# Optimization experiments

Hardware: AMD Instinct MI355X
Metric: run time of the kernel (lower is better)

The kernel has to match this reference:

```python
import jax, jax.numpy as jnp
import numpy as np

LN_EPS = 1e-5

def _layernorm(x, g, b):
    mu = jnp.mean(x, axis=-1, keepdims=True)
    var = jnp.mean(jnp.square(x - mu), axis=-1, keepdims=True)
    return (x - mu) * jax.lax.rsqrt(var + LN_EPS) * g + b

def setup_inputs() -> dict:
    key = jax.random.key(0)
    B, IN_DIM, S, D = 16384, 512, 32, 128
    ks = jax.random.split(key, 6)
    return {
        "x": jax.random.normal(ks[0], (B, IN_DIM), dtype=jnp.float32),
        "memory": jax.random.normal(ks[1], (1, S, D), dtype=jnp.float32),
        "ln_g": jnp.ones((IN_DIM,), dtype=jnp.float32),
        "ln_b": jnp.zeros((IN_DIM,), dtype=jnp.float32),
        "w_in": jax.random.normal(ks[2], (IN_DIM, D), dtype=jnp.float32) * 0.02,
        "b_in": jnp.zeros((D,), dtype=jnp.float32),
        "w_gate": jax.random.normal(ks[3], (2 * D, D), dtype=jnp.float32) * 0.02,
        "b_gate": jnp.zeros((D,), dtype=jnp.float32),
    }

def reference(x, memory, ln_g, ln_b, w_in, b_in, w_gate, b_gate):
    B = x.shape[0]
    mem = memory[0]                                   # [S, D]
    S, D = mem.shape
    x_proj = _layernorm(x, ln_g, ln_b) @ w_in + b_in  # [B, D]
    scores = x_proj @ mem.T                           # [B, S]
    probs = jax.nn.softmax(scores, axis=-1)           # [B, S]
    # read path
    read_content = probs @ mem                        # [B, D]
    # write path
    mem_b = jnp.broadcast_to(mem, (B, S, D))
    xp_b = jnp.broadcast_to(x_proj[:, None, :], (B, S, D))
    gate_in = jnp.concatenate([mem_b, xp_b], axis=-1)              # [B, S, 2D]
    update_gate = jax.nn.sigmoid(gate_in @ w_gate + b_gate)        # [B, S, D]
    write_info = probs[:, :, None] * x_proj[:, None, :]            # [B, S, D]
    avg_gate = jnp.mean(update_gate, axis=0, keepdims=True)        # [1, S, D]
    avg_write = jnp.mean(write_info, axis=0, keepdims=True)        # [1, S, D]
    new_memory = memory * (1.0 - avg_gate) + avg_write * avg_gate  # [1, S, D]
    return read_content, jax.lax.stop_gradient(new_memory)
```

## Files before the change

kernel.cpp:

```cpp
#include <hip/hip_runtime.h>
#include <stdint.h>

typedef __attribute__((ext_vector_type(8))) short bfrag_t;
typedef __attribute__((ext_vector_type(4))) float floatx4;

#define WFRAG_OFF   0
#define GB_OFF      294912
#define BU_OFF      311296
#define BS_OFF      311808
#define MEMFRAG_OFF 311936
#define ACC_OFF     327680
#define NBLK        512

#define M_A     0
#define M_XPF   32768
#define M_U     40960
#define M_SC    57344
#define M_PR    61440
#define M_PRT   63488
#define M_LDS   65536

__device__ __forceinline__ unsigned short f2bf(float f) {
    unsigned u = __float_as_uint(f);
    u += 0x7fffu + ((u >> 16) & 1u);
    return (unsigned short)(u >> 16);
}
__device__ __forceinline__ float sigm(float v) {
    return __builtin_amdgcn_rcpf(1.0f + __expf(-v));
}
__device__ __forceinline__ void writefrag(unsigned short* wf, int k, int n, float v) {
    int kt = k >> 5, kk = k & 31;
    int lane = (n & 15) | ((kk >> 3) << 4);
    wf[(((kt * 18) + (n >> 4)) * 64 + lane) * 8 + (kk & 7)] = f2bf(v);
}

__global__ __launch_bounds__(256) void prep_kernel(
    const float* __restrict__ memv, const float* __restrict__ w_in,
    const float* __restrict__ b_in, const float* __restrict__ w_gate,
    const float* __restrict__ b_gate, unsigned char* __restrict__ ws)
{
    int bid = blockIdx.x, t = threadIdx.x;
    unsigned short* wfrag = (unsigned short*)(ws + WFRAG_OFF);
    const float* wg2 = w_gate + 128 * 128;

    if (bid < 256) {
        __shared__ float wrow[2][128];
        int k0 = bid * 2;
        wrow[t >> 7][t & 127] = w_in[(size_t)(k0 + (t >> 7)) * 128 + (t & 127)];
        __syncthreads();
        for (int kl = 0; kl < 2; ++kl) {
            int k = k0 + kl;
            float v;
            if (t < 128) {
                v = wrow[kl][t];
            } else {
                int d = t - 128;
                float acc = 0.f;
                #pragma unroll 16
                for (int j = 0; j < 128; ++j) acc += wrow[kl][j] * wg2[j * 128 + d];
                v = acc;
            }
            writefrag(wfrag, k, t, v);
            if (t < 32) {
                float acc = 0.f;
                #pragma unroll 16
                for (int d = 0; d < 128; ++d) acc += wrow[kl][d] * memv[t * 128 + d];
                writefrag(wfrag, k, 256 + t, acc);
            }
        }
    } else if (bid < 272) {
        int idx = (bid - 256) * 256 + t;
        int s = idx >> 7, d = idx & 127;
        float acc = b_gate[d];
        #pragma unroll 16
        for (int k = 0; k < 128; ++k) acc += memv[s * 128 + k] * w_gate[k * 128 + d];
        ((float*)(ws + GB_OFF))[idx] = acc;
    } else {
        if (t < 128) {
            float acc = 0.f;
            #pragma unroll 16
            for (int j = 0; j < 128; ++j) acc += b_in[j] * wg2[j * 128 + t];
            ((float*)(ws + BU_OFF))[t] = acc;
        }
        if (t < 32) {
            float acc = 0.f;
            #pragma unroll 16
            for (int d = 0; d < 128; ++d) acc += b_in[d] * memv[t * 128 + d];
            ((float*)(ws + BS_OFF))[t] = acc;
        }
        unsigned short* mfr = (unsigned short*)(ws + MEMFRAG_OFF);
        for (int idx = t; idx < 4096; idx += 256) {
            int s = idx >> 7, d = idx & 127;
            mfr[((d >> 4) * 64 + ((d & 15) | (((s >> 3) & 3) << 4))) * 8 + (s & 7)]
                = f2bf(memv[idx]);
        }
    }
}

__global__ __launch_bounds__(512, 4) void main_kernel(
    const float* __restrict__ x,
    const float* __restrict__ ln_g, const float* __restrict__ ln_b,
    const float* __restrict__ b_in, unsigned char* __restrict__ ws,
    float* __restrict__ out)
{
    __shared__ char smem[M_LDS] __attribute__((aligned(16)));

    int tid = threadIdx.x;
    int w = tid >> 6, l = tid & 63;
    int lane_lo = l & 15, lane_hi = l >> 4;
    int row_base = blockIdx.x * 32;

    const float4* x4 = (const float4*)x;
    float4 g0 = ((const float4*)ln_g)[l];
    float4 g1 = ((const float4*)ln_g)[l + 64];
    float4 q0 = ((const float4*)ln_b)[l];
    float4 q1 = ((const float4*)ln_b)[l + 64];
    #pragma unroll
    for (int i = 0; i < 4; ++i) {
        int r = w * 4 + i;
        float4 xa = x4[(size_t)(row_base + r) * 128 + l];
        float4 xb = x4[(size_t)(row_base + r) * 128 + 64 + l];
        float s1 = xa.x + xa.y + xa.z + xa.w + xb.x + xb.y + xb.z + xb.w;
        float s2 = xa.x*xa.x + xa.y*xa.y + xa.z*xa.z + xa.w*xa.w
                 + xb.x*xb.x + xb.y*xb.y + xb.z*xb.z + xb.w*xb.w;
        #pragma unroll
        for (int m = 1; m < 64; m <<= 1) {
            s1 += __shfl_xor(s1, m);
            s2 += __shfl_xor(s2, m);
        }
        float mu = s1 * (1.f / 512.f);
        float var = s2 * (1.f / 512.f) - mu * mu;
        float rs = rsqrtf(var + 1e-5f);
        float ya0 = (xa.x - mu) * rs * g0.x + q0.x;
        float ya1 = (xa.y - mu) * rs * g0.y + q0.y;
        float ya2 = (xa.z - mu) * rs * g0.z + q0.z;
        float ya3 = (xa.w - mu) * rs * g0.w + q0.w;
        float yb0 = (xb.x - mu) * rs * g1.x + q1.x;
        float yb1 = (xb.y - mu) * rs * g1.y + q1.y;
        float yb2 = (xb.z - mu) * rs * g1.z + q1.z;
        float yb3 = (xb.w - mu) * rs * g1.w + q1.w;
        unsigned long long pa =
            (unsigned long long)f2bf(ya0) | ((unsigned long long)f2bf(ya1) << 16) |
            ((unsigned long long)f2bf(ya2) << 32) | ((unsigned long long)f2bf(ya3) << 48);
        unsigned long long pb =
            (unsigned long long)f2bf(yb0) | ((unsigned long long)f2bf(yb1) << 16) |
            ((unsigned long long)f2bf(yb2) << 32) | ((unsigned long long)f2bf(yb3) << 48);
        int sw = (r & 7) << 4;
        *(unsigned long long*)(smem + M_A + ((r * 1024 + l * 8) ^ sw)) = pa;
        *(unsigned long long*)(smem + M_A + ((r * 1024 + 512 + l * 8) ^ sw)) = pb;
    }
    __syncthreads();

    int nf = (w < 2) ? 3 : 2;
    int nts[3] = {w, w + 8, 16 + w};

    const bfrag_t* wf = (const bfrag_t*)(ws + WFRAG_OFF);
    int swa = (l & 7) << 4;
    int ab0 = lane_lo * 1024 + (lane_hi << 4);
    int ab1 = (16 + lane_lo) * 1024 + (lane_hi << 4);

    floatx4 acc[3][2];
    #pragma unroll
    for (int i = 0; i < 3; ++i)
        #pragma unroll
        for (int mt = 0; mt < 2; ++mt)
            acc[i][mt] = (floatx4){0.f, 0.f, 0.f, 0.f};

    bfrag_t acur0, acur1, anxt0, anxt1, bcur[3], bnxt[3];
    acur0 = *(const bfrag_t*)(smem + M_A + (ab0 ^ swa));
    acur1 = *(const bfrag_t*)(smem + M_A + (ab1 ^ swa));
    #pragma unroll
    for (int i = 0; i < 3; ++i)
        if (i < nf) bcur[i] = wf[(0 * 18 + nts[i]) * 64 + l];

    for (int kt = 0; kt < 16; ++kt) {
        if (kt < 15) {
            int ko = (kt + 1) * 64;
            anxt0 = *(const bfrag_t*)(smem + M_A + ((ab0 + ko) ^ swa));
            anxt1 = *(const bfrag_t*)(smem + M_A + ((ab1 + ko) ^ swa));
            #pragma unroll
            for (int i = 0; i < 3; ++i)
                if (i < nf) bnxt[i] = wf[((kt + 1) * 18 + nts[i]) * 64 + l];
        }
        #pragma unroll
        for (int i = 0; i < 3; ++i) {
            if (i < nf) {
                acc[i][0] = __builtin_amdgcn_mfma_f32_16x16x32_bf16(acur0, bcur[i], acc[i][0], 0, 0, 0);
                acc[i][1] = __builtin_amdgcn_mfma_f32_16x16x32_bf16(acur1, bcur[i], acc[i][1], 0, 0, 0);
            }
        }
        acur0 = anxt0; acur1 = anxt1;
        #pragma unroll
        for (int i = 0; i < 3; ++i)
            if (i < nf) bcur[i] = bnxt[i];
    }

    {
        const float* bu = (const float*)(ws + BU_OFF);
        const float* bs = (const float*)(ws + BS_OFF);
        #pragma unroll
        for (int i = 0; i < 3; ++i) {
            if (i < nf) {
                int n = nts[i] * 16 + lane_lo;
                #pragma unroll
                for (int mt = 0; mt < 2; ++mt) {
                    #pragma unroll
                    for (int r4 = 0; r4 < 4; ++r4) {
                        int row = mt * 16 + lane_hi * 4 + r4;
                        float v = acc[i][mt][r4];
                        if (i == 0) {
                            float val = v + b_in[n];
                            int addr = M_XPF +
                                (((n >> 4) * 64 + ((n & 15) | ((row >> 3) << 4))) * 8
                                 + (row & 7)) * 2;
                            *(unsigned short*)(smem + addr) = f2bf(val);
                        } else if (i == 1) {
                            int d = n - 128;
                            *(float*)(smem + M_U + (row * 128 + d) * 4) = v + bu[d];
                        } else {
                            int s = n - 256;
                            *(float*)(smem + M_SC + (row * 32 + s) * 4) = v + bs[s];
                        }
                    }
                }
            }
        }
    }
    __syncthreads();

    #pragma unroll
    for (int i = 0; i < 4; ++i) {
        int r = w * 4 + i;
        int s = l & 31;
        float sc = *(const float*)(smem + M_SC + (r * 32 + s) * 4);
        float mx = sc;
        #pragma unroll
        for (int m = 1; m < 32; m <<= 1) mx = fmaxf(mx, __shfl_xor(mx, m));
        float e = __expf(sc - mx);
        float sum = e;
        #pragma unroll
        for (int m = 1; m < 32; m <<= 1) sum += __shfl_xor(sum, m);
        float p = e * __builtin_amdgcn_rcpf(sum);
        if (l < 32) {
            unsigned short pb = f2bf(p);
            *(unsigned short*)(smem + M_PR +
                (((r >> 4) * 64 + ((r & 15) + 16 * (s >> 3))) * 8 + (s & 7)) * 2) = pb;
            *(unsigned short*)(smem + M_PRT +
                (((s >> 4) * 64 + ((s & 15) + 16 * (r >> 3))) * 8 + (r & 7)) * 2) = pb;
        }
    }
    __syncthreads();

    float* pw = (float*)(ws + ACC_OFF + (size_t)blockIdx.x * 32768);
    {
        bfrag_t pa0 = *(const bfrag_t*)(smem + M_PR + l * 16);
        bfrag_t pa1 = *(const bfrag_t*)(smem + M_PR + 1024 + l * 16);
        bfrag_t pat0 = *(const bfrag_t*)(smem + M_PRT + l * 16);
        bfrag_t pat1 = *(const bfrag_t*)(smem + M_PRT + 1024 + l * 16);
        bfrag_t bm = ((const bfrag_t*)(ws + MEMFRAG_OFF))[w * 64 + l];
        bfrag_t bx = *(const bfrag_t*)(smem + M_XPF + (w * 64 + l) * 16);

        floatx4 r0 = (floatx4){0.f, 0.f, 0.f, 0.f};
        floatx4 r1 = (floatx4){0.f, 0.f, 0.f, 0.f};
        r0 = __builtin_amdgcn_mfma_f32_16x16x32_bf16(pa0, bm, r0, 0, 0, 0);
        r1 = __builtin_amdgcn_mfma_f32_16x16x32_bf16(pa1, bm, r1, 0, 0, 0);
        floatx4 w0 = (floatx4){0.f, 0.f, 0.f, 0.f};
        floatx4 w1 = (floatx4){0.f, 0.f, 0.f, 0.f};
        w0 = __builtin_amdgcn_mfma_f32_16x16x32_bf16(pat0, bx, w0, 0, 0, 0);
        w1 = __builtin_amdgcn_mfma_f32_16x16x32_bf16(pat1, bx, w1, 0, 0, 0);

        int nc = w * 16 + lane_lo;
        #pragma unroll
        for (int r4 = 0; r4 < 4; ++r4) {
            int row = lane_hi * 4 + r4;
            out[(size_t)(row_base + row) * 128 + nc] = r0[r4];
            out[(size_t)(row_base + row + 16) * 128 + nc] = r1[r4];
            pw[row * 128 + nc] = w0[r4];
            pw[(row + 16) * 128 + nc] = w1[r4];
        }
    }

    {
        int sbase = w * 4;
        const float* gb = (const float*)(ws + GB_OFF);
        float* pg = pw + 4096;
        float gbr0[4], gbr1[4], ag0[4], ag1[4];
        #pragma unroll
        for (int si = 0; si < 4; ++si) {
            gbr0[si] = gb[(sbase + si) * 128 + l];
            gbr1[si] = gb[(sbase + si) * 128 + l + 64];
            ag0[si] = 0.f; ag1[si] = 0.f;
        }
        for (int r = 0; r < 32; ++r) {
            float uv0 = *(const float*)(smem + M_U + (r * 128 + l) * 4);
            float uv1 = *(const float*)(smem + M_U + (r * 128 + l + 64) * 4);
            #pragma unroll
            for (int si = 0; si < 4; ++si) {
                ag0[si] += sigm(gbr0[si] + uv0);
                ag1[si] += sigm(gbr1[si] + uv1);
            }
        }
        #pragma unroll
        for (int si = 0; si < 4; ++si) {
            pg[(sbase + si) * 128 + l]      = ag0[si];
            pg[(sbase + si) * 128 + l + 64] = ag1[si];
        }
    }
}

__global__ __launch_bounds__(512) void fin_kernel(
    const float* __restrict__ memv, const unsigned char* __restrict__ ws,
    float* __restrict__ out2)
{
    __shared__ float4 red[2][32][16];
    int b = blockIdx.x, t = threadIdx.x;
    int f4 = t & 15, ch = t >> 4;
    const float* base = (const float*)(ws + ACC_OFF);
    int e4 = b * 16 + f4;

    float4 aw = {0.f, 0.f, 0.f, 0.f}, ag = {0.f, 0.f, 0.f, 0.f};
    #pragma unroll 4
    for (int c = ch * 16; c < ch * 16 + 16; ++c) {
        float4 a = ((const float4*)(base + (size_t)c * 8192))[e4];
        float4 g = ((const float4*)(base + (size_t)c * 8192 + 4096))[e4];
        aw.x += a.x; aw.y += a.y; aw.z += a.z; aw.w += a.w;
        ag.x += g.x; ag.y += g.y; ag.z += g.z; ag.w += g.w;
    }
    red[0][ch][f4] = aw;
    red[1][ch][f4] = ag;
    __syncthreads();
    if (t < 16) {
        float4 a = {0.f, 0.f, 0.f, 0.f}, g = {0.f, 0.f, 0.f, 0.f};
        #pragma unroll
        for (int c = 0; c < 32; ++c) {
            float4 ra = red[0][c][t], rg = red[1][c][t];
            a.x += ra.x; a.y += ra.y; a.z += ra.z; a.w += ra.w;
            g.x += rg.x; g.y += rg.y; g.z += rg.z; g.w += rg.w;
        }
        const float4 m4 = ((const float4*)memv)[b * 16 + t];
        float4 o;
        float s = 1.f / 16384.f;
        float gx = g.x * s, gy = g.y * s, gz = g.z * s, gw = g.w * s;
        o.x = m4.x * (1.f - gx) + a.x * s * gx;
        o.y = m4.y * (1.f - gy) + a.y * s * gy;
        o.z = m4.z * (1.f - gz) + a.z * s * gz;
        o.w = m4.w * (1.f - gw) + a.w * s * gw;
        ((float4*)out2)[b * 16 + t] = o;
    }
}

extern "C" void kernel_launch(void* const* d_in, const int* in_sizes, int n_in,
                              void* d_out, int out_size, void* d_ws, size_t ws_size,
                              hipStream_t stream)
{
    (void)in_sizes; (void)n_in; (void)out_size; (void)ws_size;
    const float* x      = (const float*)d_in[0];
    const float* memv   = (const float*)d_in[1];
    const float* ln_g   = (const float*)d_in[2];
    const float* ln_b   = (const float*)d_in[3];
    const float* w_in   = (const float*)d_in[4];
    const float* b_in   = (const float*)d_in[5];
    const float* w_gate = (const float*)d_in[6];
    const float* b_gate = (const float*)d_in[7];
    float* out = (float*)d_out;
    unsigned char* ws = (unsigned char*)d_ws;

    hipLaunchKernelGGL(prep_kernel, dim3(273), dim3(256), 0, stream,
                       memv, w_in, b_in, w_gate, b_gate, ws);
    hipLaunchKernelGGL(main_kernel, dim3(NBLK), dim3(512), 0, stream,
                       x, ln_g, ln_b, b_in, ws, out);
    hipLaunchKernelGGL(fin_kernel, dim3(64), dim3(512), 0, stream,
                       memv, ws, out + 2097152);
}
```

Measured before the change: 48.69 us.

## Hoist global loads earlier and deepen MFMA operand prefetch to two stages

Issues all x row loads up front, then prefetches the first two weight fragments and the bias values before the layernorm math, so global latency overlaps the reductions. The GEMM loop now prefetches both A and B fragments two k-steps ahead instead of one. The memory fragment, xproj fragment and gate-bias loads are hoisted above the softmax phase, and the sigmoid accumulation loop is unrolled by 4. This raises register pressure under launch_bounds(512,4), which could cause spills or lower occupancy.

Measured after the change: 49.15 us. No clear change (+0.9%).

```diff
diff --git a/kernel.cpp b/kernel.cpp
--- a/kernel.cpp
+++ b/kernel.cpp
@@ -110,19 +110,42 @@
     int lane_lo = l & 15, lane_hi = l >> 4;
     int row_base = blockIdx.x * 32;
 
+    int nf = (w < 2) ? 3 : 2;
+    int nts[3] = {w, w + 8, 16 + w};
+    const bfrag_t* wf = (const bfrag_t*)(ws + WFRAG_OFF);
+
     const float4* x4 = (const float4*)x;
     float4 g0 = ((const float4*)ln_g)[l];
     float4 g1 = ((const float4*)ln_g)[l + 64];
     float4 q0 = ((const float4*)ln_b)[l];
     float4 q1 = ((const float4*)ln_b)[l + 64];
+
+    float4 xa[4], xb[4];
     #pragma unroll
     for (int i = 0; i < 4; ++i) {
         int r = w * 4 + i;
-        float4 xa = x4[(size_t)(row_base + r) * 128 + l];
-        float4 xb = x4[(size_t)(row_base + r) * 128 + 64 + l];
-        float s1 = xa.x + xa.y + xa.z + xa.w + xb.x + xb.y + xb.z + xb.w;
-        float s2 = xa.x*xa.x + xa.y*xa.y + xa.z*xa.z + xa.w*xa.w
-                 + xb.x*xb.x + xb.y*xb.y + xb.z*xb.z + xb.w*xb.w;
+        xa[i] = x4[(size_t)(row_base + r) * 128 + l];
+        xb[i] = x4[(size_t)(row_base + r) * 128 + 64 + l];
+    }
+
+    bfrag_t bcur[3], bnxt[3], bfar[3];
+    #pragma unroll
+    for (int i = 0; i < 3; ++i) {
+        if (i < nf) {
+            bcur[i] = wf[(0 * 18 + nts[i]) * 64 + l];
+            bnxt[i] = wf[(1 * 18 + nts[i]) * 64 + l];
+        }
+    }
+    float bin_v = b_in[w * 16 + lane_lo];
+    float bu_v  = ((const float*)(ws + BU_OFF))[w * 16 + lane_lo];
+    float bs_v  = (w < 2) ? ((const float*)(ws + BS_OFF))[w * 16 + lane_lo] : 0.f;
+
+    #pragma unroll
+    for (int i = 0; i < 4; ++i) {
+        int r = w * 4 + i;
+        float s1 = xa[i].x + xa[i].y + xa[i].z + xa[i].w + xb[i].x + xb[i].y + xb[i].z + xb[i].w;
+        float s2 = xa[i].x*xa[i].x + xa[i].y*xa[i].y + xa[i].z*xa[i].z + xa[i].w*xa[i].w
+                 + xb[i].x*xb[i].x + xb[i].y*xb[i].y + xb[i].z*xb[i].z + xb[i].w*xb[i].w;
         #pragma unroll
         for (int m = 1; m < 64; m <<= 1) {
             s1 += __shfl_xor(s1, m);
@@ -131,14 +154,14 @@
         float mu = s1 * (1.f / 512.f);
         float var = s2 * (1.f / 512.f) - mu * mu;
         float rs = rsqrtf(var + 1e-5f);
-        float ya0 = (xa.x - mu) * rs * g0.x + q0.x;
-        float ya1 = (xa.y - mu) * rs * g0.y + q0.y;
-        float ya2 = (xa.z - mu) * rs * g0.z + q0.z;
-        float ya3 = (xa.w - mu) * rs * g0.w + q0.w;
-        float yb0 = (xb.x - mu) * rs * g1.x + q1.x;
-        float yb1 = (xb.y - mu) * rs * g1.y + q1.y;
-        float yb2 = (xb.z - mu) * rs * g1.z + q1.z;
-        float yb3 = (xb.w - mu) * rs * g1.w + q1.w;
+        float ya0 = (xa[i].x - mu) * rs * g0.x + q0.x;
+        float ya1 = (xa[i].y - mu) * rs * g0.y + q0.y;
+        float ya2 = (xa[i].z - mu) * rs * g0.z + q0.z;
+        float ya3 = (xa[i].w - mu) * rs * g0.w + q0.w;
+        float yb0 = (xb[i].x - mu) * rs * g1.x + q1.x;
+        float yb1 = (xb[i].y - mu) * rs * g1.y + q1.y;
+        float yb2 = (xb[i].z - mu) * rs * g1.z + q1.z;
+        float yb3 = (xb[i].w - mu) * rs * g1.w + q1.w;
         unsigned long long pa =
             (unsigned long long)f2bf(ya0) | ((unsigned long long)f2bf(ya1) << 16) |
             ((unsigned long long)f2bf(ya2) << 32) | ((unsigned long long)f2bf(ya3) << 48);
@@ -151,10 +174,6 @@
     }
     __syncthreads();
 
-    int nf = (w < 2) ? 3 : 2;
-    int nts[3] = {w, w + 8, 16 + w};
-
-    const bfrag_t* wf = (const bfrag_t*)(ws + WFRAG_OFF);
     int swa = (l & 7) << 4;
     int ab0 = lane_lo * 1024 + (lane_hi << 4);
     int ab1 = (16 + lane_lo) * 1024 + (lane_hi << 4);
@@ -166,21 +185,20 @@
         for (int mt = 0; mt < 2; ++mt)
             acc[i][mt] = (floatx4){0.f, 0.f, 0.f, 0.f};
 
-    bfrag_t acur0, acur1, anxt0, anxt1, bcur[3], bnxt[3];
+    bfrag_t acur0, acur1, anxt0, anxt1, afar0, afar1;
     acur0 = *(const bfrag_t*)(smem + M_A + (ab0 ^ swa));
     acur1 = *(const bfrag_t*)(smem + M_A + (ab1 ^ swa));
-    #pragma unroll
-    for (int i = 0; i < 3; ++i)
-        if (i < nf) bcur[i] = wf[(0 * 18 + nts[i]) * 64 + l];
+    anxt0 = *(const bfrag_t*)(smem + M_A + ((ab0 + 64) ^ swa));
+    anxt1 = *(const bfrag_t*)(smem + M_A + ((ab1 + 64) ^ swa));
 
     for (int kt = 0; kt < 16; ++kt) {
-        if (kt < 15) {
-            int ko = (kt + 1) * 64;
-            anxt0 = *(const bfrag_t*)(smem + M_A + ((ab0 + ko) ^ swa));
-            anxt1 = *(const bfrag_t*)(smem + M_A + ((ab1 + ko) ^ swa));
+        if (kt < 14) {
+            int ko = (kt + 2) * 64;
+            afar0 = *(const bfrag_t*)(smem + M_A + ((ab0 + ko) ^ swa));
+            afar1 = *(const bfrag_t*)(smem + M_A + ((ab1 + ko) ^ swa));
             #pragma unroll
             for (int i = 0; i < 3; ++i)
-                if (i < nf) bnxt[i] = wf[((kt + 1) * 18 + nts[i]) * 64 + l];
+                if (i < nf) bfar[i] = wf[((kt + 2) * 18 + nts[i]) * 64 + l];
         }
         #pragma unroll
         for (int i = 0; i < 3; ++i) {
@@ -189,37 +207,35 @@
                 acc[i][1] = __builtin_amdgcn_mfma_f32_16x16x32_bf16(acur1, bcur[i], acc[i][1], 0, 0, 0);
             }
         }
-        acur0 = anxt0; acur1 = anxt1;
+        acur0 = anxt0; acur1 = anxt1; anxt0 = afar0; anxt1 = afar1;
         #pragma unroll
         for (int i = 0; i < 3; ++i)
-            if (i < nf) bcur[i] = bnxt[i];
+            if (i < nf) { bcur[i] = bnxt[i]; bnxt[i] = bfar[i]; }
     }
 
     {
-        const float* bu = (const float*)(ws + BU_OFF);
-        const float* bs = (const float*)(ws + BS_OFF);
         #pragma unroll
         for (int i = 0; i < 3; ++i) {
             if (i < nf) {
                 int n = nts[i] * 16 + lane_lo;
+                float bias = (i == 0) ? bin_v : ((i == 1) ? bu_v : bs_v);
                 #pragma unroll
                 for (int mt = 0; mt < 2; ++mt) {
                     #pragma unroll
                     for (int r4 = 0; r4 < 4; ++r4) {
                         int row = mt * 16 + lane_hi * 4 + r4;
-                        float v = acc[i][mt][r4];
+                        float v = acc[i][mt][r4] + bias;
                         if (i == 0) {
-                            float val = v + b_in[n];
                             int addr = M_XPF +
                                 (((n >> 4) * 64 + ((n & 15) | ((row >> 3) << 4))) * 8
                                  + (row & 7)) * 2;
-                            *(unsigned short*)(smem + addr) = f2bf(val);
+                            *(unsigned short*)(smem + addr) = f2bf(v);
                         } else if (i == 1) {
                             int d = n - 128;
-                            *(float*)(smem + M_U + (row * 128 + d) * 4) = v + bu[d];
+                            *(float*)(smem + M_U + (row * 128 + d) * 4) = v;
                         } else {
                             int s = n - 256;
-                            *(float*)(smem + M_SC + (row * 32 + s) * 4) = v + bs[s];
+                            *(float*)(smem + M_SC + (row * 32 + s) * 4) = v;
                         }
                     }
                 }
@@ -227,6 +243,17 @@
         }
     }
     __syncthreads();
+
+    bfrag_t bm = ((const bfrag_t*)(ws + MEMFRAG_OFF))[w * 64 + l];
+    bfrag_t bx = *(const bfrag_t*)(smem + M_XPF + (w * 64 + l) * 16);
+    int sbase = w * 4;
+    const float* gb = (const float*)(ws + GB_OFF);
+    float gbr0[4], gbr1[4];
+    #pragma unroll
+    for (int si = 0; si < 4; ++si) {
+        gbr0[si] = gb[(sbase + si) * 128 + l];
+        gbr1[si] = gb[(sbase + si) * 128 + l + 64];
+    }
 
     #pragma unroll
     for (int i = 0; i < 4; ++i) {
@@ -257,8 +284,6 @@
         bfrag_t pa1 = *(const bfrag_t*)(smem + M_PR + 1024 + l * 16);
         bfrag_t pat0 = *(const bfrag_t*)(smem + M_PRT + l * 16);
         bfrag_t pat1 = *(const bfrag_t*)(smem + M_PRT + 1024 + l * 16);
-        bfrag_t bm = ((const bfrag_t*)(ws + MEMFRAG_OFF))[w * 64 + l];
-        bfrag_t bx = *(const bfrag_t*)(smem + M_XPF + (w * 64 + l) * 16);
 
         floatx4 r0 = (floatx4){0.f, 0.f, 0.f, 0.f};
         floatx4 r1 = (floatx4){0.f, 0.f, 0.f, 0.f};
@@ -281,16 +306,11 @@
     }
 
     {
-        int sbase = w * 4;
-        const float* gb = (const float*)(ws + GB_OFF);
         float* pg = pw + 4096;
-        float gbr0[4], gbr1[4], ag0[4], ag1[4];
-        #pragma unroll
-        for (int si = 0; si < 4; ++si) {
-            gbr0[si] = gb[(sbase + si) * 128 + l];
-            gbr1[si] = gb[(sbase + si) * 128 + l + 64];
-            ag0[si] = 0.f; ag1[si] = 0.f;
-        }
+        float ag0[4], ag1[4];
+        #pragma unroll
+        for (int si = 0; si < 4; ++si) { ag0[si] = 0.f; ag1[si] = 0.f; }
+        #pragma unroll 4
         for (int r = 0; r < 32; ++r) {
             float uv0 = *(const float*)(smem + M_U + (r * 128 + l) * 4);
             float uv1 = *(const float*)(smem + M_U + (r * 128 + l + 64) * 4);
```
